# Kernel tuning notes

Hardware: AMD Instinct MI355X
Metric: run time of the kernel (lower is better)

The kernel has to match this reference:

```python
import jax, jax.numpy as jnp
import numpy as np

N_NODES = 50000
N_EDGES = 1_600_000
D_IN = 128
D_HID = 128
D_OUT = 128


def _linear_init(key, out_dim, in_dim, bias=True):
    k1, k2 = jax.random.split(key)
    bound = 1.0 / np.sqrt(in_dim)
    W = jax.random.uniform(k1, (out_dim, in_dim), jnp.float32, -bound, bound)
    if bias:
        b = jax.random.uniform(k2, (out_dim,), jnp.float32, -bound, bound)
        return W, b
    return W, None


def _leconv_params(key, in_dim, out_dim):
    k1, k2, k3 = jax.random.split(key, 3)
    W1, b1 = _linear_init(k1, out_dim, in_dim, bias=True)   # lin1 (applied to x_j)
    W2, _ = _linear_init(k2, out_dim, in_dim, bias=False)   # lin2 (applied to x_i)
    W3, b3 = _linear_init(k3, out_dim, in_dim, bias=True)   # lin3 (skip on x_i)
    return W1, b1, W2, W3, b3


def setup_inputs() -> dict:
    key = jax.random.key(0)
    kx, ke, kw, k_in, k_mid, k_out = jax.random.split(key, 6)
    x = jax.random.normal(kx, (N_NODES, D_IN), jnp.float32)
    edge_index = jax.random.randint(ke, (2, N_EDGES), 0, N_NODES, dtype=jnp.int32)
    edge_weight = jax.random.uniform(kw, (N_EDGES,), jnp.float32)
    iW1, ib1, iW2, iW3, ib3 = _leconv_params(k_in, D_IN, D_HID)
    mW1, mb1, mW2, mW3, mb3 = _leconv_params(k_mid, D_HID, D_HID)
    oW1, ob1, oW2, oW3, ob3 = _leconv_params(k_out, D_HID, D_OUT)
    return {
        "x": x, "edge_index": edge_index, "edge_weight": edge_weight,
        "in_W1": iW1, "in_b1": ib1, "in_W2": iW2, "in_W3": iW3, "in_b3": ib3,
        "mid_W1": mW1, "mid_b1": mb1, "mid_W2": mW2, "mid_W3": mW3, "mid_b3": mb3,
        "out_W1": oW1, "out_b1": ob1, "out_W2": oW2, "out_W3": oW3, "out_b3": ob3,
        "number_of_layers": 4,
    }


def _leconv(h, src, dst, ew, W1, b1, W2, W3, b3):
    # out_i = sum_{j->i} e_ji * ((W1 x_j + b1) - W2 x_i) + (W3 x_i + b3)
    a = h @ W1.T + b1          # [N, F_out]
    b = h @ W2.T               # [N, F_out]
    msg = ew[:, None] * (a[src] - b[dst])              # [E, F_out]
    agg = jax.ops.segment_sum(msg, dst, num_segments=h.shape[0])
    return agg + h @ W3.T + b3


def _lrelu(x):
    return jnp.where(x >= 0, x, 0.1 * x)


def reference(x, edge_index, edge_weight,
              in_W1, in_b1, in_W2, in_W3, in_b3,
              mid_W1, mid_b1, mid_W2, mid_W3, mid_b3,
              out_W1, out_b1, out_W2, out_W3, out_b3,
              number_of_layers):
    src, dst = edge_index[0], edge_index[1]
    h = _lrelu(_leconv(x, src, dst, edge_weight, in_W1, in_b1, in_W2, in_W3, in_b3))
    for _ in range(number_of_layers - 2):  # shared inner weights, as in the torch module
        h = _lrelu(_leconv(h, src, dst, edge_weight, mid_W1, mid_b1, mid_W2, mid_W3, mid_b3))
    h = _lrelu(_leconv(h, src, dst, edge_weight, out_W1, out_b1, out_W2, out_W3, out_b3))
    return jax.nn.sigmoid(h)
```

## Files before the change

kernel.cpp:

```cpp
#include <hip/hip_runtime.h>
#include <hip/hip_fp16.h>
#include <math.h>

#define D 128
#define CSH 13
#define BSH 9
#define NB_MAX 128

typedef _Float16 f16;
typedef __attribute__((ext_vector_type(8))) _Float16 f16x8;
typedef __attribute__((ext_vector_type(4))) float f32x4;


__global__ __launch_bounds__(256) void binA_count(
    const int* __restrict__ dst, int* __restrict__ bucketCount, int E)
{
    __shared__ int hist[NB_MAX];
    int tid = threadIdx.x;
    if (tid < NB_MAX) hist[tid] = 0;
    __syncthreads();
    int base = blockIdx.x * 4096;
    for (int i = tid; i < 4096; i += 256) {
        int e = base + i;
        if (e < E) atomicAdd(&hist[dst[e] >> BSH], 1);
    }
    __syncthreads();
    if (tid < NB_MAX && hist[tid]) atomicAdd(&bucketCount[tid], hist[tid]);
}

__global__ void bucket_scan(
    const int* __restrict__ bucketCount, int* __restrict__ bucketBase,
    int* __restrict__ bucketCursor, int* __restrict__ row_off,
    int NBUC, int E, int N)
{
    if (threadIdx.x == 0 && blockIdx.x == 0) {
        int p = 0;
        for (int b = 0; b < NBUC; ++b) {
            bucketBase[b] = p; bucketCursor[b] = p; p += bucketCount[b];
        }
        bucketBase[NBUC] = p;
        row_off[N] = E;
    }
}

__global__ __launch_bounds__(256) void binA_scatter(
    const int* __restrict__ src, const int* __restrict__ dst,
    const float* __restrict__ ew, int* __restrict__ bucketCursor,
    int4* __restrict__ binned, int E)
{
    __shared__ int hist[NB_MAX], off[NB_MAX], cbase[NB_MAX];
    int tid = threadIdx.x;
    if (tid < NB_MAX) { hist[tid] = 0; off[tid] = 0; }
    __syncthreads();
    int base = blockIdx.x * 4096;
    for (int i = tid; i < 4096; i += 256) {
        int e = base + i;
        if (e < E) atomicAdd(&hist[dst[e] >> BSH], 1);
    }
    __syncthreads();
    if (tid < NB_MAX && hist[tid])
        cbase[tid] = atomicAdd(&bucketCursor[tid], hist[tid]);
    __syncthreads();
    for (int i = tid; i < 4096; i += 256) {
        int e = base + i;
        if (e < E) {
            int d = dst[e];
            int b = d >> BSH;
            int pos = cbase[b] + atomicAdd(&off[b], 1);
            binned[pos] = make_int4(src[e], __float_as_int(ew[e]), d, 0);
        }
    }
}

__global__ __launch_bounds__(1024) void binB_kernel(
    const int4* __restrict__ binned, const int* __restrict__ bucketBase,
    int2* __restrict__ edge_s, int* __restrict__ row_off,
    float* __restrict__ sdeg, int N, int nchunk)
{
    __shared__ int hist[4096];
    __shared__ int cur[4096];
    __shared__ float sdl[512];
    __shared__ int wsum[16];

    int b    = blockIdx.x;
    int tid  = threadIdx.x;
    int ebeg = bucketBase[b], eend = bucketBase[b + 1];
    int node0 = b << BSH;
    int nib   = min(512, N - node0);

    for (int i = tid; i < 4096; i += 1024) hist[i] = 0;
    for (int i = tid; i < 512; i += 1024) sdl[i] = 0.f;
    __syncthreads();

    for (int e = ebeg + tid; e < eend; e += 1024) {
        int4 ed = binned[e];
        int dl = ed.z - node0;
        int ch = ((unsigned)ed.x) >> CSH;
        atomicAdd(&hist[dl * nchunk + ch], 1);
        atomicAdd(&sdl[dl], __int_as_float(ed.y));
    }
    __syncthreads();

    int t4 = tid * 4;
    int h0 = hist[t4], h1 = hist[t4 + 1], h2 = hist[t4 + 2], h3 = hist[t4 + 3];
    int sum = h0 + h1 + h2 + h3;
    int lane = tid & 63, wid = tid >> 6;
    int x = sum;
    #pragma unroll
    for (int o = 1; o < 64; o <<= 1) { int t = __shfl_up(x, o); if (lane >= o) x += t; }
    if (lane == 63) wsum[wid] = x;
    __syncthreads();
    if (tid < 16) {
        int y = wsum[tid];
        #pragma unroll
        for (int o = 1; o < 16; o <<= 1) { int t = __shfl_up(y, o, 16); if (tid >= o) y += t; }
        wsum[tid] = y;
    }
    __syncthreads();
    int excl = (wid ? wsum[wid - 1] : 0) + x - sum;
    cur[t4] = excl; cur[t4 + 1] = excl + h0;
    cur[t4 + 2] = excl + h0 + h1; cur[t4 + 3] = excl + h0 + h1 + h2;
    __syncthreads();

    for (int dl = tid; dl < nib; dl += 1024) {
        row_off[node0 + dl] = ebeg + cur[dl * nchunk];
        sdeg[node0 + dl]    = sdl[dl];
    }
    __syncthreads();

    for (int e = ebeg + tid; e < eend; e += 1024) {
        int4 ed = binned[e];
        int dl = ed.z - node0;
        int ch = ((unsigned)ed.x) >> CSH;
        int pos = ebeg + atomicAdd(&cur[dl * nchunk + ch], 1);
        edge_s[pos] = make_int2(ed.x, ed.y);
    }
}

__global__ __launch_bounds__(256) void pack_kernel(
    const float* __restrict__ W1, const float* __restrict__ W2,
    const float* __restrict__ W3, f16* __restrict__ Wp)
{
    int idx = blockIdx.x * 256 + threadIdx.x;
    if (idx >= 6144) return;
    int lane = idx & 63;
    int t    = idx >> 6;
    int ks   = t & 3;
    int mot  = t >> 2;
    int m    = mot >> 3;
    int ot   = mot & 7;
    const float* W = (m == 0) ? W1 : (m == 1) ? W2 : W3;
    int o  = ot * 16 + (lane & 15);
    int kb = ks * 32 + (lane >> 4) * 8;
    f16x8 hi, lo;
    #pragma unroll
    for (int j = 0; j < 8; ++j) {
        float v = W[(size_t)o * D + kb + j];
        f16 hh = (f16)v;
        hi[j] = hh;
        lo[j] = (f16)(v - (float)hh);
    }
    size_t base = (size_t)ks * 24576 + (size_t)mot * 1024 + (size_t)lane * 8;
    *(f16x8*)&Wp[base]       = hi;
    *(f16x8*)&Wp[base + 512] = lo;
}


__global__ __launch_bounds__(256, 2) void gemm_kernel(
    const float* __restrict__ in, const f16* __restrict__ Wp,
    const float* __restrict__ b1, const float* __restrict__ b3,
    const float* __restrict__ sdeg, float* __restrict__ aA,
    float* __restrict__ aB, float* __restrict__ base_out,
    int N, int ntiles, int gridb)
{
    int tid  = threadIdx.x;
    int lane = tid & 63;
    int wid  = tid >> 6;
    int col  = lane & 15;
    int g    = lane >> 4;

    f16x8 w[3][2][4][2];
    #pragma unroll
    for (int m = 0; m < 3; ++m)
        #pragma unroll
        for (int oti = 0; oti < 2; ++oti) {
            int mot = m * 8 + wid * 2 + oti;
            #pragma unroll
            for (int ks = 0; ks < 4; ++ks) {
                const f16* p = Wp + (size_t)ks * 24576 + (size_t)mot * 1024 + (size_t)lane * 8;
                w[m][oti][ks][0] = *(const f16x8*)p;
                w[m][oti][ks][1] = *(const f16x8*)(p + 512);
            }
        }

    float bi1[2], bi3[2];
    #pragma unroll
    for (int oti = 0; oti < 2; ++oti) {
        int o = (wid * 2 + oti) * 16 + col;
        bi1[oti] = b1[o];
        bi3[oti] = b3[o];
    }

    for (int t = blockIdx.x; t < ntiles; t += gridb) {
        int n0   = t * 16;
        int nrow = n0 + col;

        f32x4 acc[3][2];
        #pragma unroll
        for (int m = 0; m < 3; ++m)
            #pragma unroll
            for (int oti = 0; oti < 2; ++oti)
                acc[m][oti] = (f32x4){0.f, 0.f, 0.f, 0.f};

        #pragma unroll
        for (int ks = 0; ks < 4; ++ks) {
            float av[8];
            if (nrow < N) {
                float4 a0 = *(const float4*)&in[(size_t)nrow * D + ks * 32 + g * 8];
                float4 a1 = *(const float4*)&in[(size_t)nrow * D + ks * 32 + g * 8 + 4];
                av[0] = a0.x; av[1] = a0.y; av[2] = a0.z; av[3] = a0.w;
                av[4] = a1.x; av[5] = a1.y; av[6] = a1.z; av[7] = a1.w;
            } else {
                #pragma unroll
                for (int j = 0; j < 8; ++j) av[j] = 0.f;
            }
            f16x8 ahi, alo;
            #pragma unroll
            for (int j = 0; j < 8; ++j) {
                f16 hh = (f16)av[j];
                ahi[j] = hh;
                alo[j] = (f16)(av[j] - (float)hh);
            }
            #pragma unroll
            for (int m = 0; m < 3; ++m)
                #pragma unroll
                for (int oti = 0; oti < 2; ++oti) {
                    acc[m][oti] = __builtin_amdgcn_mfma_f32_16x16x32_f16(ahi, w[m][oti][ks][0], acc[m][oti], 0, 0, 0);
                    acc[m][oti] = __builtin_amdgcn_mfma_f32_16x16x32_f16(alo, w[m][oti][ks][0], acc[m][oti], 0, 0, 0);
                    acc[m][oti] = __builtin_amdgcn_mfma_f32_16x16x32_f16(ahi, w[m][oti][ks][1], acc[m][oti], 0, 0, 0);
                }
        }

        float* ah = (wid < 2) ? aA : aB;
        #pragma unroll
        for (int oti = 0; oti < 2; ++oti) {
            int o  = (wid * 2 + oti) * 16 + col;
            int oh = o & 63;
            #pragma unroll
            for (int r = 0; r < 4; ++r) {
                int node = n0 + g * 4 + r;
                if (node < N) {
                    float sv   = sdeg[node];
                    float aval = acc[0][oti][r] + bi1[oti];
                    float bval = acc[2][oti][r] + bi3[oti] - sv * acc[1][oti][r];
                    ah[(size_t)node * 64 + oh]     = aval;
                    base_out[(size_t)node * D + o] = bval;
                }
            }
        }
    }
}


__global__ __launch_bounds__(256) void agg_kernel(
    const float* __restrict__ aA, const float* __restrict__ aB,
    const float* __restrict__ base, const int* __restrict__ row_off,
    const int2* __restrict__ edge_s, float* __restrict__ out, int N, int last)
{
    int lane = threadIdx.x & 63;
    int wid  = threadIdx.x >> 6;
    int nA   = blockIdx.x * 8 + wid * 2;
    int nB   = nA + 1;
    if (nA >= N) return;
    bool hasB = (nB < N);

    const float* aH = (lane < 32) ? aA : aB;
    int fo = (lane & 31) * 2;
    int l2 = lane * 2;

    float2 accA = *(const float2*)&base[(size_t)nA * D + l2];
    int eA = row_off[nA], endA = row_off[nA + 1];
    float2 accB = make_float2(0.f, 0.f);
    int eB = 0, endB = 0;
    if (hasB) {
        accB = *(const float2*)&base[(size_t)nB * D + l2];
        eB = row_off[nB]; endB = row_off[nB + 1];
    }

    while (eA + 4 <= endA && eB + 4 <= endB) {
        int2 m[8];
        #pragma unroll
        for (int i = 0; i < 4; ++i) m[i] = edge_s[eA + i];
        #pragma unroll
        for (int i = 0; i < 4; ++i) m[4 + i] = edge_s[eB + i];
        float2 v[8];
        #pragma unroll
        for (int i = 0; i < 8; ++i)
            v[i] = *(const float2*)&aH[(size_t)m[i].x * 64 + fo];
        #pragma unroll
        for (int i = 0; i < 4; ++i) {
            float wgt = __int_as_float(m[i].y);
            accA.x = fmaf(wgt, v[i].x, accA.x);
            accA.y = fmaf(wgt, v[i].y, accA.y);
        }
        #pragma unroll
        for (int i = 0; i < 4; ++i) {
            float wgt = __int_as_float(m[4 + i].y);
            accB.x = fmaf(wgt, v[4 + i].x, accB.x);
            accB.y = fmaf(wgt, v[4 + i].y, accB.y);
        }
        eA += 4; eB += 4;
    }

    auto finish = [&](int e, int end, float2& acc) {
        for (; e + 8 <= end; e += 8) {
            int2 m[8];
            #pragma unroll
            for (int i = 0; i < 8; ++i) m[i] = edge_s[e + i];
            float2 v[8];
            #pragma unroll
            for (int i = 0; i < 8; ++i)
                v[i] = *(const float2*)&aH[(size_t)m[i].x * 64 + fo];
            #pragma unroll
            for (int i = 0; i < 8; ++i) {
                float wgt = __int_as_float(m[i].y);
                acc.x = fmaf(wgt, v[i].x, acc.x);
                acc.y = fmaf(wgt, v[i].y, acc.y);
            }
        }
        for (; e < end; ++e) {
            int2 m = edge_s[e];
            float2 v = *(const float2*)&aH[(size_t)m.x * 64 + fo];
            float wgt = __int_as_float(m.y);
            acc.x = fmaf(wgt, v.x, acc.x);
            acc.y = fmaf(wgt, v.y, acc.y);
        }
    };
    finish(eA, endA, accA);
    if (hasB) finish(eB, endB, accB);

    accA.x = accA.x >= 0.f ? accA.x : 0.1f * accA.x;
    accA.y = accA.y >= 0.f ? accA.y : 0.1f * accA.y;
    if (last) {
        accA.x = 1.f / (1.f + __expf(-accA.x));
        accA.y = 1.f / (1.f + __expf(-accA.y));
    }
    *(float2*)&out[(size_t)nA * D + l2] = accA;
    if (hasB) {
        accB.x = accB.x >= 0.f ? accB.x : 0.1f * accB.x;
        accB.y = accB.y >= 0.f ? accB.y : 0.1f * accB.y;
        if (last) {
            accB.x = 1.f / (1.f + __expf(-accB.x));
            accB.y = 1.f / (1.f + __expf(-accB.y));
        }
        *(float2*)&out[(size_t)nB * D + l2] = accB;
    }
}


extern "C" void kernel_launch(void* const* d_in, const int* in_sizes, int n_in,
                              void* d_out, int out_size, void* d_ws, size_t ws_size,
                              hipStream_t stream) {
    const float* x   = (const float*)d_in[0];
    const int*   ei  = (const int*)d_in[1];
    const float* ew  = (const float*)d_in[2];
    const float* iW1 = (const float*)d_in[3];
    const float* ib1 = (const float*)d_in[4];
    const float* iW2 = (const float*)d_in[5];
    const float* iW3 = (const float*)d_in[6];
    const float* ib3 = (const float*)d_in[7];
    const float* mW1 = (const float*)d_in[8];
    const float* mb1 = (const float*)d_in[9];
    const float* mW2 = (const float*)d_in[10];
    const float* mW3 = (const float*)d_in[11];
    const float* mb3 = (const float*)d_in[12];
    const float* oW1 = (const float*)d_in[13];
    const float* ob1 = (const float*)d_in[14];
    const float* oW2 = (const float*)d_in[15];
    const float* oW3 = (const float*)d_in[16];
    const float* ob3 = (const float*)d_in[17];

    int N = in_sizes[0] / D;
    int E = in_sizes[2];
    const int* src = ei;
    const int* dst = ei + E;
    int nchunk = (N + (1 << CSH) - 1) >> CSH;
    int NBUC   = (N + (1 << BSH) - 1) >> BSH;

    char* wsp = (char*)d_ws;
    size_t off = 0;
    auto alloc = [&](size_t bytes) -> void* {
        void* p = wsp + off;
        off += (bytes + 255) & ~(size_t)255;
        return p;
    };
    float* h        = (float*)alloc((size_t)N * D * 4);
    float* base     = (float*)alloc((size_t)N * D * 4);
    float* aA       = (float*)alloc((size_t)N * 64 * 4);
    float* aB       = (float*)alloc((size_t)N * 64 * 4);
    float* sdeg     = (float*)alloc((size_t)N * 4);
    int*   row_off  = (int*)alloc((size_t)(N + 1) * 4);
    int2*  edge_s   = (int2*)alloc((size_t)E * 8);
    int*   bucketCount  = (int*)alloc((size_t)(NBUC + 1) * 4);
    int*   bucketBase   = (int*)alloc((size_t)(NBUC + 1) * 4);
    int*   bucketCursor = (int*)alloc((size_t)(NBUC + 1) * 4);
    f16*   Wp       = (f16*)alloc((size_t)3 * 98304 * 2);

    int4* binned = (int4*)h;

    hipMemsetAsync(bucketCount, 0, (size_t)(NBUC + 1) * 4, stream);

    int ablocks  = (N + 7) / 8;
    int ntiles   = (N + 15) / 16;
    int gridb    = 512;
    int abblocks = (E + 4095) / 4096;

    pack_kernel<<<24, 256, 0, stream>>>(iW1, iW2, iW3, Wp);
    pack_kernel<<<24, 256, 0, stream>>>(mW1, mW2, mW3, Wp + 98304);
    pack_kernel<<<24, 256, 0, stream>>>(oW1, oW2, oW3, Wp + 2 * 98304);

    binA_count<<<abblocks, 256, 0, stream>>>(dst, bucketCount, E);
    bucket_scan<<<1, 64, 0, stream>>>(bucketCount, bucketBase, bucketCursor,
                                      row_off, NBUC, E, N);
    binA_scatter<<<abblocks, 256, 0, stream>>>(src, dst, ew, bucketCursor,
                                               binned, E);
    binB_kernel<<<NBUC, 1024, 0, stream>>>(binned, bucketBase, edge_s,
                                           row_off, sdeg, N, nchunk);

    gemm_kernel<<<gridb, 256, 0, stream>>>(x, Wp, ib1, ib3, sdeg, aA, aB, base, N, ntiles, gridb);
    agg_kernel<<<ablocks, 256, 0, stream>>>(aA, aB, base, row_off, edge_s, h, N, 0);
    for (int l = 0; l < 2; ++l) {
        gemm_kernel<<<gridb, 256, 0, stream>>>(h, Wp + 98304, mb1, mb3, sdeg, aA, aB, base, N, ntiles, gridb);
        agg_kernel<<<ablocks, 256, 0, stream>>>(aA, aB, base, row_off, edge_s, h, N, 0);
    }
    gemm_kernel<<<gridb, 256, 0, stream>>>(h, Wp + 2 * 98304, ob1, ob3, sdeg, aA, aB, base, N, ntiles, gridb);
    agg_kernel<<<ablocks, 256, 0, stream>>>(aA, aB, base, row_off, edge_s, (float*)d_out, N, 1);
}
```

Before: 678.5 us.

## Use finer source chunks in edge binning and grid-stride persistent aggregation

Shrinks the source-chunk shift in the per-destination edge sort so each destination's edges are grouped into finer source-id ranges, improving gather locality in the aggregation kernel. The histogram and cursor arrays grow to 13312 entries, and each thread now scans 13 entries. The aggregation kernel becomes a persistent grid-stride loop over node pairs with a fixed 2048-block grid, cutting block launch overhead. The larger shared-memory footprint lowers binning occupancy and assumes nchunk fits the enlarged histogram.

```diff
diff --git a/kernel.cpp b/kernel.cpp
--- a/kernel.cpp
+++ b/kernel.cpp
@@ -3,9 +3,10 @@
 #include <math.h>
 
 #define D 128
-#define CSH 13
+#define CSH 11
 #define BSH 9
 #define NB_MAX 128
+#define NHMAX 13312
 
 typedef _Float16 f16;
 typedef __attribute__((ext_vector_type(8))) _Float16 f16x8;
@@ -77,8 +78,8 @@
     int2* __restrict__ edge_s, int* __restrict__ row_off,
     float* __restrict__ sdeg, int N, int nchunk)
 {
-    __shared__ int hist[4096];
-    __shared__ int cur[4096];
+    __shared__ int hist[NHMAX];
+    __shared__ int cur[NHMAX];
     __shared__ float sdl[512];
     __shared__ int wsum[16];
 
@@ -88,8 +89,8 @@
     int node0 = b << BSH;
     int nib   = min(512, N - node0);
 
-    for (int i = tid; i < 4096; i += 1024) hist[i] = 0;
-    for (int i = tid; i < 512; i += 1024) sdl[i] = 0.f;
+    for (int i = tid; i < NHMAX; i += 1024) hist[i] = 0;
+    if (tid < 512) sdl[tid] = 0.f;
     __syncthreads();
 
     for (int e = ebeg + tid; e < eend; e += 1024) {
@@ -101,11 +102,13 @@
     }
     __syncthreads();
 
-    int t4 = tid * 4;
-    int h0 = hist[t4], h1 = hist[t4 + 1], h2 = hist[t4 + 2], h3 = hist[t4 + 3];
-    int sum = h0 + h1 + h2 + h3;
+    int base_i = tid * 13;
+    int v[13];
+    int tot = 0;
+    #pragma unroll
+    for (int j = 0; j < 13; ++j) { v[j] = hist[base_i + j]; tot += v[j]; }
     int lane = tid & 63, wid = tid >> 6;
-    int x = sum;
+    int x = tot;
     #pragma unroll
     for (int o = 1; o < 64; o <<= 1) { int t = __shfl_up(x, o); if (lane >= o) x += t; }
     if (lane == 63) wsum[wid] = x;
@@ -117,9 +120,9 @@
         wsum[tid] = y;
     }
     __syncthreads();
-    int excl = (wid ? wsum[wid - 1] : 0) + x - sum;
-    cur[t4] = excl; cur[t4 + 1] = excl + h0;
-    cur[t4 + 2] = excl + h0 + h1; cur[t4 + 3] = excl + h0 + h1 + h2;
+    int p = (wid ? wsum[wid - 1] : 0) + x - tot;
+    #pragma unroll
+    for (int j = 0; j < 13; ++j) { cur[base_i + j] = p; p += v[j]; }
     __syncthreads();
 
     for (int dl = tid; dl < nib; dl += 1024) {
@@ -265,95 +268,97 @@
 __global__ __launch_bounds__(256) void agg_kernel(
     const float* __restrict__ aA, const float* __restrict__ aB,
     const float* __restrict__ base, const int* __restrict__ row_off,
-    const int2* __restrict__ edge_s, float* __restrict__ out, int N, int last)
+    const int2* __restrict__ edge_s, float* __restrict__ out,
+    int N, int last, int npairs, int gridb)
 {
     int lane = threadIdx.x & 63;
     int wid  = threadIdx.x >> 6;
-    int nA   = blockIdx.x * 8 + wid * 2;
-    int nB   = nA + 1;
-    if (nA >= N) return;
-    bool hasB = (nB < N);
-
     const float* aH = (lane < 32) ? aA : aB;
     int fo = (lane & 31) * 2;
     int l2 = lane * 2;
 
-    float2 accA = *(const float2*)&base[(size_t)nA * D + l2];
-    int eA = row_off[nA], endA = row_off[nA + 1];
-    float2 accB = make_float2(0.f, 0.f);
-    int eB = 0, endB = 0;
-    if (hasB) {
-        accB = *(const float2*)&base[(size_t)nB * D + l2];
-        eB = row_off[nB]; endB = row_off[nB + 1];
-    }
-
-    while (eA + 4 <= endA && eB + 4 <= endB) {
-        int2 m[8];
-        #pragma unroll
-        for (int i = 0; i < 4; ++i) m[i] = edge_s[eA + i];
-        #pragma unroll
-        for (int i = 0; i < 4; ++i) m[4 + i] = edge_s[eB + i];
-        float2 v[8];
-        #pragma unroll
-        for (int i = 0; i < 8; ++i)
-            v[i] = *(const float2*)&aH[(size_t)m[i].x * 64 + fo];
-        #pragma unroll
-        for (int i = 0; i < 4; ++i) {
-            float wgt = __int_as_float(m[i].y);
-            accA.x = fmaf(wgt, v[i].x, accA.x);
-            accA.y = fmaf(wgt, v[i].y, accA.y);
-        }
-        #pragma unroll
-        for (int i = 0; i < 4; ++i) {
-            float wgt = __int_as_float(m[4 + i].y);
-            accB.x = fmaf(wgt, v[4 + i].x, accB.x);
-            accB.y = fmaf(wgt, v[4 + i].y, accB.y);
-        }
-        eA += 4; eB += 4;
-    }
-
-    auto finish = [&](int e, int end, float2& acc) {
-        for (; e + 8 <= end; e += 8) {
+    for (int pr = blockIdx.x * 4 + wid; pr < npairs; pr += gridb * 4) {
+        int nA = pr * 2;
+        int nB = nA + 1;
+        bool hasB = (nB < N);
+
+        float2 accA = *(const float2*)&base[(size_t)nA * D + l2];
+        int eA = row_off[nA], endA = row_off[nA + 1];
+        float2 accB = make_float2(0.f, 0.f);
+        int eB = 0, endB = 0;
+        if (hasB) {
+            accB = *(const float2*)&base[(size_t)nB * D + l2];
+            eB = row_off[nB]; endB = row_off[nB + 1];
+        }
+
+        while (eA + 4 <= endA && eB + 4 <= endB) {
             int2 m[8];
             #pragma unroll
-            for (int i = 0; i < 8; ++i) m[i] = edge_s[e + i];
+            for (int i = 0; i < 4; ++i) m[i] = edge_s[eA + i];
+            #pragma unroll
+            for (int i = 0; i < 4; ++i) m[4 + i] = edge_s[eB + i];
             float2 v[8];
             #pragma unroll
             for (int i = 0; i < 8; ++i)
                 v[i] = *(const float2*)&aH[(size_t)m[i].x * 64 + fo];
             #pragma unroll
-            for (int i = 0; i < 8; ++i) {
+            for (int i = 0; i < 4; ++i) {
                 float wgt = __int_as_float(m[i].y);
-                acc.x = fmaf(wgt, v[i].x, acc.x);
-                acc.y = fmaf(wgt, v[i].y, acc.y);
-            }
-        }
-        for (; e < end; ++e) {
-            int2 m = edge_s[e];
-            float2 v = *(const float2*)&aH[(size_t)m.x * 64 + fo];
-            float wgt = __int_as_float(m.y);
-            acc.x = fmaf(wgt, v.x, acc.x);
-            acc.y = fmaf(wgt, v.y, acc.y);
-        }
-    };
-    finish(eA, endA, accA);
-    if (hasB) finish(eB, endB, accB);
-
-    accA.x = accA.x >= 0.f ? accA.x : 0.1f * accA.x;
-    accA.y = accA.y >= 0.f ? accA.y : 0.1f * accA.y;
-    if (last) {
-        accA.x = 1.f / (1.f + __expf(-accA.x));
-        accA.y = 1.f / (1.f + __expf(-accA.y));
-    }
-    *(float2*)&out[(size_t)nA * D + l2] = accA;
-    if (hasB) {
-        accB.x = accB.x >= 0.f ? accB.x : 0.1f * accB.x;
-        accB.y = accB.y >= 0.f ? accB.y : 0.1f * accB.y;
+                accA.x = fmaf(wgt, v[i].x, accA.x);
+                accA.y = fmaf(wgt, v[i].y, accA.y);
+            }
+            #pragma unroll
+            for (int i = 0; i < 4; ++i) {
+                float wgt = __int_as_float(m[4 + i].y);
+                accB.x = fmaf(wgt, v[4 + i].x, accB.x);
+                accB.y = fmaf(wgt, v[4 + i].y, accB.y);
+            }
+            eA += 4; eB += 4;
+        }
+
+        auto finish = [&](int e, int end, float2& acc) {
+            for (; e + 8 <= end; e += 8) {
+                int2 m[8];
+                #pragma unroll
+                for (int i = 0; i < 8; ++i) m[i] = edge_s[e + i];
+                float2 v[8];
+                #pragma unroll
+                for (int i = 0; i < 8; ++i)
+                    v[i] = *(const float2*)&aH[(size_t)m[i].x * 64 + fo];
+                #pragma unroll
+                for (int i = 0; i < 8; ++i) {
+                    float wgt = __int_as_float(m[i].y);
+                    acc.x = fmaf(wgt, v[i].x, acc.x);
+                    acc.y = fmaf(wgt, v[i].y, acc.y);
+                }
+            }
+            for (; e < end; ++e) {
+                int2 m = edge_s[e];
+                float2 v = *(const float2*)&aH[(size_t)m.x * 64 + fo];
+                float wgt = __int_as_float(m.y);
+                acc.x = fmaf(wgt, v.x, acc.x);
+                acc.y = fmaf(wgt, v.y, acc.y);
+            }
+        };
+        finish(eA, endA, accA);
+        if (hasB) finish(eB, endB, accB);
+
+        accA.x = accA.x >= 0.f ? accA.x : 0.1f * accA.x;
+        accA.y = accA.y >= 0.f ? accA.y : 0.1f * accA.y;
         if (last) {
-            accB.x = 1.f / (1.f + __expf(-accB.x));
-            accB.y = 1.f / (1.f + __expf(-accB.y));
-        }
-        *(float2*)&out[(size_t)nB * D + l2] = accB;
+            accA.x = 1.f / (1.f + __expf(-accA.x));
+            accA.y = 1.f / (1.f + __expf(-accA.y));
+        }
+        *(float2*)&out[(size_t)nA * D + l2] = accA;
+        if (hasB) {
+            accB.x = accB.x >= 0.f ? accB.x : 0.1f * accB.x;
+            accB.y = accB.y >= 0.f ? accB.y : 0.1f * accB.y;
+            if (last) {
+                accB.x = 1.f / (1.f + __expf(-accB.x));
+                accB.y = 1.f / (1.f + __expf(-accB.y));
+            }
+            *(float2*)&out[(size_t)nB * D + l2] = accB;
+        }
     }
 }
 
@@ -410,7 +415,8 @@
 
     hipMemsetAsync(bucketCount, 0, (size_t)(NBUC + 1) * 4, stream);
 
-    int ablocks  = (N + 7) / 8;
+    int npairs   = (N + 1) / 2;
+    int aggb     = 2048;
     int ntiles   = (N + 15) / 16;
     int gridb    = 512;
     int abblocks = (E + 4095) / 4096;
@@ -428,11 +434,11 @@
                                            row_off, sdeg, N, nchunk);
 
     gemm_kernel<<<gridb, 256, 0, stream>>>(x, Wp, ib1, ib3, sdeg, aA, aB, base, N, ntiles, gridb);
-    agg_kernel<<<ablocks, 256, 0, stream>>>(aA, aB, base, row_off, edge_s, h, N, 0);
+    agg_kernel<<<aggb, 256, 0, stream>>>(aA, aB, base, row_off, edge_s, h, N, 0, npairs, aggb);
     for (int l = 0; l < 2; ++l) {
         gemm_kernel<<<gridb, 256, 0, stream>>>(h, Wp + 98304, mb1, mb3, sdeg, aA, aB, base, N, ntiles, gridb);
-        agg_kernel<<<ablocks, 256, 0, stream>>>(aA, aB, base, row_off, edge_s, h, N, 0);
+        agg_kernel<<<aggb, 256, 0, stream>>>(aA, aB, base, row_off, edge_s, h, N, 0, npairs, aggb);
     }
     gemm_kernel<<<gridb, 256, 0, stream>>>(h, Wp + 2 * 98304, ob1, ob3, sdeg, aA, aB, base, N, ntiles, gridb);
-    agg_kernel<<<ablocks, 256, 0, stream>>>(aA, aB, base, row_off, edge_s, (float*)d_out, N, 1);
-}
+    agg_kernel<<<aggb, 256, 0, stream>>>(aA, aB, base, row_off, edge_s, (float*)d_out, N, 1, npairs, aggb);
+}
```

New measurement: 702.5 us. +3.5%, slower.
